# Kernel tuning notes

Measured on AMD Instinct MI355X. Metric: run time of the kernel, lower is better.

Reference implementation:

```python
import jax, jax.numpy as jnp
import numpy as np

INPUT_DIM = 1024
NUM_HEADS = 16


def setup_inputs() -> dict:
    key = jax.random.key(0)
    k1, k2, k3, k4, k5, k6, k7, k8 = jax.random.split(key, 8)
    bs, seq, dm = 2, 2048, INPUT_DIM
    scale = 1.0 / np.sqrt(dm)
    return {
        "input": jax.random.normal(k1, (bs, seq, dm), dtype=jnp.float32),
        "mask": jax.random.randint(k2, (bs, seq), 0, 2, dtype=jnp.int32),
        "Wq": jax.random.normal(k3, (dm, dm), dtype=jnp.float32) * scale,
        "bq": jax.random.normal(k4, (dm,), dtype=jnp.float32) * 0.01,
        "Wk": jax.random.normal(k5, (dm, dm), dtype=jnp.float32) * scale,
        "bk": jax.random.normal(k6, (dm,), dtype=jnp.float32) * 0.01,
        "Wv": jax.random.normal(k7, (dm, dm), dtype=jnp.float32) * scale,
        "bv": jax.random.normal(k8, (dm,), dtype=jnp.float32) * 0.01,
    }


def reference(input, mask, Wq, bq, Wk, bk, Wv, bv):
    bs, seq, dm = input.shape
    h = NUM_HEADS
    d = dm // h
    # projections: x @ W^T + b (torch Linear convention)
    Q = (input @ Wq.T + bq).reshape(bs, seq, h, d).transpose(0, 2, 1, 3)
    K = (input @ Wk.T + bk).reshape(bs, seq, h, d).transpose(0, 2, 1, 3)
    V = (input @ Wv.T + bv).reshape(bs, seq, h, d).transpose(0, 2, 1, 3)
    # raw scores [bs, h, seq, seq]
    scores = jnp.einsum("bhqd,bhkd->bhqk", Q, K)
    m = mask.astype(jnp.float32).reshape(bs, 1, 1, seq)
    # mask_logits is applied BEFORE the 1/sqrt(d) scaling, as in source
    scores = scores * m + (1.0 - m) * (-1e30)
    scores = scores * (1.0 / np.sqrt(d))
    attn = jax.nn.softmax(scores, axis=-1)  # dropout = identity at eval
    out = jnp.einsum("bhqk,bhkd->bhqd", attn, V)
    return out.transpose(0, 2, 1, 3).reshape(bs, seq, dm)
```

## Files before the change

kernel.cpp:

```cpp
#include <hip/hip_runtime.h>
#include <stdint.h>
#include <stddef.h>

#define SEQ 2048
#define DM  1024
#define NH  16
#define BS  2

typedef __attribute__((ext_vector_type(8)))  __bf16 bf16x8;
typedef __attribute__((ext_vector_type(4)))  __bf16 bf16x4;
typedef __attribute__((ext_vector_type(4)))  float  floatx4;
typedef __attribute__((ext_vector_type(16))) float  floatx16;
typedef __attribute__((ext_vector_type(4)))  unsigned int uintx4;
typedef __attribute__((ext_vector_type(4)))  unsigned short ushortx4;

#if __has_builtin(__builtin_amdgcn_exp2f)
#define EXP2(x) __builtin_amdgcn_exp2f(x)
#else
#define EXP2(x) __expf((x) * 0.6931471805599453f)
#endif

#define QSCALE 0.18033688011112042f

#define GLDS(g, s) __builtin_amdgcn_global_load_lds( \
    (const __attribute__((address_space(1))) void*)(g), \
    (__attribute__((address_space(3))) void*)(s), 16, 0, 0)

__device__ inline unsigned short f2bf(float f) {
  union { float f; unsigned int u; } a; a.f = f;
  unsigned int u = a.u;
  return (unsigned short)((u + 0x7fffu + ((u >> 16) & 1u)) >> 16);
}

__device__ inline bf16x8 ldb8(const unsigned short* p) { return *(const bf16x8*)p; }

__global__ __launch_bounds__(256) void prep(
    const float* __restrict__ x, const float* __restrict__ wq,
    const float* __restrict__ wk, const float* __restrict__ wv,
    const int* __restrict__ mask,
    unsigned short* __restrict__ Xb, unsigned short* __restrict__ Wb,
    unsigned short* __restrict__ mb01) {
  const int bid = blockIdx.x, t = threadIdx.x;
  if (bid < 7168) {
    const float* src; unsigned short* dst; int base;
    if (bid < 4096)      { src = x;  dst = Xb;            base = bid; }
    else if (bid < 5120) { src = wq; dst = Wb;            base = bid - 4096; }
    else if (bid < 6144) { src = wk; dst = Wb + 1048576;  base = bid - 5120; }
    else                 { src = wv; dst = Wb + 2097152;  base = bid - 6144; }
    const int i = base * 256 + t;
    floatx4 v = ((const floatx4*)src)[i];
    ushortx4 o;
    o.x = f2bf(v.x); o.y = f2bf(v.y); o.z = f2bf(v.z); o.w = f2bf(v.w);
    ((ushortx4*)dst)[i] = o;
  } else {
    const int i = (bid - 7168) * 256 + t;
    mb01[i] = mask[i] ? 0x3F80 : 0;
  }
}

__global__ __launch_bounds__(256, 3) void gemm_qkv(
    const unsigned short* __restrict__ Xb, const unsigned short* __restrict__ Wb,
    const float* __restrict__ bq, const float* __restrict__ bk, const float* __restrict__ bv,
    const int* __restrict__ mask,
    unsigned short* __restrict__ Qb, unsigned short* __restrict__ Kb,
    unsigned short* __restrict__ Vt)
{
  __shared__ alignas(16) unsigned short LB[16384];
  const int t = threadIdx.x;
  const int w = t >> 6, l = t & 63;
  const int lm = l & 15, lq = l >> 4;
  const int z = blockIdx.z;
  const size_t m0 = (size_t)blockIdx.y * 128;
  const size_t n0 = (size_t)blockIdx.x * 128;
  const unsigned short* W = Wb + (size_t)z * (1024 * 1024);
  const float* bias = (z == 0) ? bq : ((z == 1) ? bk : bv);
  const float sc = (z == 0) ? QSCALE : 1.0f;

  const int c0 = t, c1 = 256 + t;
  const int row0 = c0 >> 2, row1 = c1 >> 2;
  const int kq0 = (c0 & 3) ^ ((row0 >> 1) & 3);
  const int kq1 = (c1 & 3) ^ ((row1 >> 1) & 3);
  const unsigned short* gA0 = Xb + (m0 + row0) * 1024 + kq0 * 8;
  const unsigned short* gA1 = Xb + (m0 + row1) * 1024 + kq1 * 8;
  const unsigned short* gB0 = W + (n0 + row0) * 1024 + kq0 * 8;
  const unsigned short* gB1 = W + (n0 + row1) * 1024 + kq1 * 8;
  const int la0 = (0 * 256 + w * 64) * 8;
  const int la1 = (1 * 256 + w * 64) * 8;

  const int wr = (w >> 1) * 64, wc = (w & 1) * 64;
  const int sw = (lq ^ ((lm >> 1) & 3)) * 8;
  floatx4 acc[4][4] = {};

  GLDS(gA0, LB + la0);
  GLDS(gA1, LB + la1);
  GLDS(gB0, LB + 8192 + la0);
  GLDS(gB1, LB + 8192 + la1);
  __syncthreads();

  for (int it = 0; it < 32; ++it) {
    const int cur = it & 1;
    if (it < 31) {
      const int kn = (it + 1) * 32;
      const int nb = (cur ^ 1) * 4096;
      GLDS(gA0 + kn, LB + nb + la0);
      GLDS(gA1 + kn, LB + nb + la1);
      GLDS(gB0 + kn, LB + 8192 + nb + la0);
      GLDS(gB1 + kn, LB + 8192 + nb + la1);
    }
    const unsigned short* Ab = LB + cur * 4096;
    const unsigned short* Bb = LB + 8192 + cur * 4096;
    bf16x8 af[4], bfr[4];
#pragma unroll
    for (int i = 0; i < 4; i++) af[i] = ldb8(Ab + (wr + i * 16 + lm) * 32 + sw);
#pragma unroll
    for (int j = 0; j < 4; j++) bfr[j] = ldb8(Bb + (wc + j * 16 + lm) * 32 + sw);
#pragma unroll
    for (int i = 0; i < 4; i++)
#pragma unroll
      for (int j = 0; j < 4; j++)
        acc[i][j] = __builtin_amdgcn_mfma_f32_16x16x32_bf16(af[i], bfr[j], acc[i][j], 0, 0, 0);
    __syncthreads();
  }

  if (z < 2) {
    unsigned short* dst = (z == 0) ? Qb : Kb;
#pragma unroll
    for (int j = 0; j < 4; j++) {
      const int ncol = (int)n0 + wc + j * 16 + lm;
      const float bval = bias[ncol];
#pragma unroll
      for (int i = 0; i < 4; i++)
#pragma unroll
        for (int r = 0; r < 4; r++) {
          const int mrow = (int)m0 + wr + i * 16 + lq * 4 + r;
          dst[(size_t)mrow * 1024 + ncol] = f2bf((acc[i][j][r] + bval) * sc);
        }
    }
  } else {
    float mk[4][4];
#pragma unroll
    for (int i = 0; i < 4; i++)
#pragma unroll
      for (int r = 0; r < 4; r++)
        mk[i][r] = (float)mask[(int)m0 + wr + i * 16 + lq * 4 + r];
#pragma unroll
    for (int j = 0; j < 4; j++) {
      const int nl = wc + j * 16 + lm;
      const float bval = bias[(int)n0 + nl];
#pragma unroll
      for (int i = 0; i < 4; i++)
#pragma unroll
        for (int r = 0; r < 4; r++) {
          const int ml = wr + i * 16 + lq * 4 + r;
          LB[nl * 128 + ((((ml >> 3) ^ (nl & 15)) * 8) | (ml & 7))] =
              f2bf((acc[i][j][r] + bval) * mk[i][r]);
        }
    }
    __syncthreads();
    const int nl = t >> 1, hf = t & 1;
    const int ncol = (int)n0 + nl;
    const int hh = ncol >> 6, dc = ncol & 63;
    const int bb = (int)(m0 >> 11);
    const int s0c = ((int)m0 & 2047) + hf * 64;
    unsigned short* dstp = Vt + (size_t)((bb * 16 + hh) * 64 + dc) * SEQ + s0c;
#pragma unroll
    for (int u = 0; u < 8; ++u) {
      const int phys = (hf * 8 + u) ^ (nl & 15);
      *(uintx4*)(dstp + u * 8) = *(const uintx4*)(LB + nl * 128 + phys * 8);
    }
  }
}

__global__ __launch_bounds__(256, 3) void attn(
    const unsigned short* __restrict__ Qb, const unsigned short* __restrict__ Kb,
    const unsigned short* __restrict__ Vt, const unsigned short* __restrict__ mb01,
    float* __restrict__ out)
{
  __shared__ alignas(16) unsigned short Klds[2][4096];
  __shared__ alignas(16) unsigned short Vlds[2][4096];
  __shared__ alignas(16) unsigned short Plds[4][2048];
  __shared__ alignas(16) unsigned short Mb[2048];

  const int t = threadIdx.x, w = t >> 6, l = t & 63;
  const int ln = l & 31, h = l >> 5;
  const int bid = blockIdx.x;
  const int pp = bid & 31;
  const int b = pp >> 4, head = pp & 15;
  const int q0w = (bid >> 5) * 128 + w * 32;
  const int hoff = head * 64;

  const int sr = l >> 3;
  const int gc = (l & 7) ^ sr;
  const unsigned short* gK[2]; const unsigned short* gV[2];
#pragma unroll
  for (int s2 = 0; s2 < 2; ++s2) {
    const int row = w * 16 + s2 * 8 + sr;
    gK[s2] = Kb + (size_t)(b * SEQ + row) * DM + hoff + gc * 8;
    gV[s2] = Vt + (size_t)((b * NH + head) * 64 + row) * SEQ + gc * 8;
  }

#pragma unroll
  for (int s2 = 0; s2 < 2; ++s2) {
    GLDS(gK[s2], &Klds[0][(w * 128 + s2 * 64) * 8]);
    GLDS(gV[s2], &Vlds[0][(w * 128 + s2 * 64) * 8]);
  }

  ((uintx4*)Mb)[t] = ((const uintx4*)(mb01 + b * SEQ))[t];

  const unsigned short* Qbase = Qb + (size_t)(b * SEQ + q0w + ln) * DM + hoff + h * 8;
  bf16x8 qf[4];
#pragma unroll
  for (int c = 0; c < 4; ++c) qf[c] = ldb8(Qbase + c * 16);

  const int cc = (ln >> 1) & 3, hb = h ^ (ln & 1);
  int xoff[4];
#pragma unroll
  for (int c = 0; c < 4; ++c) xoff[c] = (c ^ cc) * 16 + hb * 8;

  unsigned short* Pw = &Plds[w][ln * 64];
  floatx16 oacc[2] = {};
  floatx16 tacc = {};

  __syncthreads();

  for (int kt = 0; kt < 32; ++kt) {
    const int cur = kt & 1;
    if (kt < 31) {
      const int k0n = (kt + 1) * 64;
#pragma unroll
      for (int s2 = 0; s2 < 2; ++s2) {
        GLDS(gK[s2] + (size_t)k0n * DM, &Klds[cur ^ 1][(w * 128 + s2 * 64) * 8]);
        GLDS(gV[s2] + k0n,              &Vlds[cur ^ 1][(w * 128 + s2 * 64) * 8]);
      }
    }
    const unsigned short* Kc = &Klds[cur][ln * 64];
    const unsigned short* Vc = &Vlds[cur][ln * 64];

    bf16x8 kfr[8], vfr[8];
#pragma unroll
    for (int i = 0; i < 8; ++i) {
      kfr[i] = ldb8(Kc + (i >> 2) * 2048 + xoff[i & 3]);
      vfr[i] = ldb8(Vc + (i >> 2) * 2048 + xoff[i & 3]);
    }

    floatx16 s[2] = {};
#pragma unroll
    for (int c = 0; c < 4; ++c) {
      s[0] = __builtin_amdgcn_mfma_f32_32x32x16_bf16(kfr[c],     qf[c], s[0], 0, 0, 0);
      s[1] = __builtin_amdgcn_mfma_f32_32x32x16_bf16(kfr[4 + c], qf[c], s[1], 0, 0, 0);
    }

#pragma unroll
    for (int kb = 0; kb < 2; ++kb)
#pragma unroll
      for (int g = 0; g < 4; ++g) {
        bf16x4 pk;
#pragma unroll
        for (int r = 0; r < 4; ++r) pk[r] = (__bf16)EXP2(s[kb][g * 4 + r]);
        *(bf16x4*)(Pw + ((4 * kb + g) ^ (ln & 7)) * 8 + h * 4) = pk;
      }

    bf16x8 pf[4];
#pragma unroll
    for (int c = 0; c < 4; ++c) pf[c] = ldb8(Pw + xoff[c]);

    const int k0 = kt * 64;
#pragma unroll
    for (int c = 0; c < 4; ++c) {
      const bf16x8 mfr = ldb8(Mb + k0 + c * 16 + h * 8);
      tacc = __builtin_amdgcn_mfma_f32_32x32x16_bf16(pf[c], mfr, tacc, 0, 0, 0);
    }

#pragma unroll
    for (int c = 0; c < 4; ++c) {
      oacc[0] = __builtin_amdgcn_mfma_f32_32x32x16_bf16(pf[c], vfr[c],     oacc[0], 0, 0, 0);
      oacc[1] = __builtin_amdgcn_mfma_f32_32x32x16_bf16(pf[c], vfr[4 + c], oacc[1], 0, 0, 0);
    }
    __syncthreads();
  }

  float* obase = out + (size_t)(b * SEQ + q0w) * DM + hoff;
#pragma unroll
  for (int r = 0; r < 16; ++r) {
    const int rq = (r & 3) + 8 * (r >> 2) + 4 * h;
    const float iv = __builtin_amdgcn_rcpf(tacc[r]);
    obase[(size_t)rq * DM + ln]      = oacc[0][r] * iv;
    obase[(size_t)rq * DM + 32 + ln] = oacc[1][r] * iv;
  }
}

extern "C" void kernel_launch(void* const* d_in, const int* in_sizes, int n_in,
                              void* d_out, int out_size, void* d_ws, size_t ws_size,
                              hipStream_t stream) {
  const float* x   = (const float*)d_in[0];
  const int*   msk = (const int*)d_in[1];
  const float* Wq  = (const float*)d_in[2];
  const float* bq  = (const float*)d_in[3];
  const float* Wk  = (const float*)d_in[4];
  const float* bk  = (const float*)d_in[5];
  const float* Wv  = (const float*)d_in[6];
  const float* bv  = (const float*)d_in[7];
  float* out = (float*)d_out;

  unsigned short* ws = (unsigned short*)d_ws;
  unsigned short* Xb = ws;
  unsigned short* Wb = Xb + (size_t)4096 * 1024;
  unsigned short* Qb = Wb + (size_t)3 * 1024 * 1024;
  unsigned short* Kb = Qb + (size_t)4096 * 1024;
  unsigned short* Vt = Kb + (size_t)4096 * 1024;
  unsigned short* mb01 = Vt + (size_t)4096 * 1024;

  prep<<<7184, 256, 0, stream>>>(x, Wq, Wk, Wv, msk, Xb, Wb, mb01);

  gemm_qkv<<<dim3(8, 32, 3), 256, 0, stream>>>(Xb, Wb, bq, bk, bv, msk, Qb, Kb, Vt);

  attn<<<512, 256, 0, stream>>>(Qb, Kb, Vt, mb01, out);
}
```

Baseline: 170.5 us.

## Software-pipeline QK^T one tile ahead with triple-buffered K/V LDS

Moves the attention loop to a three-stage K/V LDS ring and starts loads two tiles ahead. The QK^T MFMAs for the next tile are issued in the same iteration as the exp/P store and the PV MFMAs of the current tile, so matrix work can overlap the transcendental and LDS phases. K and V fragments are now read from LDS right before use rather than in one batch. In exchange, LDS use grows, launch bounds drop from 3 to 2 blocks per CU, register pressure rises from the extra score accumulators, and the last iteration does one wasted QK^T on a stale buffer.

```diff
diff --git a/kernel.cpp b/kernel.cpp
--- a/kernel.cpp
+++ b/kernel.cpp
@@ -171,13 +171,13 @@
   }
 }
 
-__global__ __launch_bounds__(256, 3) void attn(
+__global__ __launch_bounds__(256, 2) void attn(
     const unsigned short* __restrict__ Qb, const unsigned short* __restrict__ Kb,
     const unsigned short* __restrict__ Vt, const unsigned short* __restrict__ mb01,
     float* __restrict__ out)
 {
-  __shared__ alignas(16) unsigned short Klds[2][4096];
-  __shared__ alignas(16) unsigned short Vlds[2][4096];
+  __shared__ alignas(16) unsigned short Klds[3][4096];
+  __shared__ alignas(16) unsigned short Vlds[3][4096];
   __shared__ alignas(16) unsigned short Plds[4][2048];
   __shared__ alignas(16) unsigned short Mb[2048];
 
@@ -201,8 +201,10 @@
 
 #pragma unroll
   for (int s2 = 0; s2 < 2; ++s2) {
-    GLDS(gK[s2], &Klds[0][(w * 128 + s2 * 64) * 8]);
-    GLDS(gV[s2], &Vlds[0][(w * 128 + s2 * 64) * 8]);
+    GLDS(gK[s2],                  &Klds[0][(w * 128 + s2 * 64) * 8]);
+    GLDS(gV[s2],                  &Vlds[0][(w * 128 + s2 * 64) * 8]);
+    GLDS(gK[s2] + (size_t)64 * DM, &Klds[1][(w * 128 + s2 * 64) * 8]);
+    GLDS(gV[s2] + 64,              &Vlds[1][(w * 128 + s2 * 64) * 8]);
   }
 
   ((uintx4*)Mb)[t] = ((const uintx4*)(mb01 + b * SEQ))[t];
@@ -223,31 +225,33 @@
 
   __syncthreads();
 
+  floatx16 scur[2] = {};
+#pragma unroll
+  for (int c = 0; c < 4; ++c) {
+    const unsigned short* Kc = &Klds[0][ln * 64];
+    scur[0] = __builtin_amdgcn_mfma_f32_32x32x16_bf16(ldb8(Kc + xoff[c]),        qf[c], scur[0], 0, 0, 0);
+    scur[1] = __builtin_amdgcn_mfma_f32_32x32x16_bf16(ldb8(Kc + 2048 + xoff[c]), qf[c], scur[1], 0, 0, 0);
+  }
+
+  int cur = 0, nxt = 1, fut = 2;
   for (int kt = 0; kt < 32; ++kt) {
-    const int cur = kt & 1;
-    if (kt < 31) {
-      const int k0n = (kt + 1) * 64;
+    if (kt < 30) {
+      const int k0n = (kt + 2) * 64;
 #pragma unroll
       for (int s2 = 0; s2 < 2; ++s2) {
-        GLDS(gK[s2] + (size_t)k0n * DM, &Klds[cur ^ 1][(w * 128 + s2 * 64) * 8]);
-        GLDS(gV[s2] + k0n,              &Vlds[cur ^ 1][(w * 128 + s2 * 64) * 8]);
+        GLDS(gK[s2] + (size_t)k0n * DM, &Klds[fut][(w * 128 + s2 * 64) * 8]);
+        GLDS(gV[s2] + k0n,              &Vlds[fut][(w * 128 + s2 * 64) * 8]);
       }
     }
-    const unsigned short* Kc = &Klds[cur][ln * 64];
-    const unsigned short* Vc = &Vlds[cur][ln * 64];
-
-    bf16x8 kfr[8], vfr[8];
-#pragma unroll
-    for (int i = 0; i < 8; ++i) {
-      kfr[i] = ldb8(Kc + (i >> 2) * 2048 + xoff[i & 3]);
-      vfr[i] = ldb8(Vc + (i >> 2) * 2048 + xoff[i & 3]);
-    }
-
-    floatx16 s[2] = {};
-#pragma unroll
-    for (int c = 0; c < 4; ++c) {
-      s[0] = __builtin_amdgcn_mfma_f32_32x32x16_bf16(kfr[c],     qf[c], s[0], 0, 0, 0);
-      s[1] = __builtin_amdgcn_mfma_f32_32x32x16_bf16(kfr[4 + c], qf[c], s[1], 0, 0, 0);
+
+    floatx16 snext[2] = {};
+    {
+      const unsigned short* Kc = &Klds[nxt][ln * 64];
+#pragma unroll
+      for (int c = 0; c < 4; ++c) {
+        snext[0] = __builtin_amdgcn_mfma_f32_32x32x16_bf16(ldb8(Kc + xoff[c]),        qf[c], snext[0], 0, 0, 0);
+        snext[1] = __builtin_amdgcn_mfma_f32_32x32x16_bf16(ldb8(Kc + 2048 + xoff[c]), qf[c], snext[1], 0, 0, 0);
+      }
     }
 
 #pragma unroll
@@ -256,7 +260,7 @@
       for (int g = 0; g < 4; ++g) {
         bf16x4 pk;
 #pragma unroll
-        for (int r = 0; r < 4; ++r) pk[r] = (__bf16)EXP2(s[kb][g * 4 + r]);
+        for (int r = 0; r < 4; ++r) pk[r] = (__bf16)EXP2(scur[kb][g * 4 + r]);
         *(bf16x4*)(Pw + ((4 * kb + g) ^ (ln & 7)) * 8 + h * 4) = pk;
       }
 
@@ -271,12 +275,18 @@
       tacc = __builtin_amdgcn_mfma_f32_32x32x16_bf16(pf[c], mfr, tacc, 0, 0, 0);
     }
 
-#pragma unroll
-    for (int c = 0; c < 4; ++c) {
-      oacc[0] = __builtin_amdgcn_mfma_f32_32x32x16_bf16(pf[c], vfr[c],     oacc[0], 0, 0, 0);
-      oacc[1] = __builtin_amdgcn_mfma_f32_32x32x16_bf16(pf[c], vfr[4 + c], oacc[1], 0, 0, 0);
-    }
+    {
+      const unsigned short* Vc = &Vlds[cur][ln * 64];
+#pragma unroll
+      for (int c = 0; c < 4; ++c) {
+        oacc[0] = __builtin_amdgcn_mfma_f32_32x32x16_bf16(pf[c], ldb8(Vc + xoff[c]),        oacc[0], 0, 0, 0);
+        oacc[1] = __builtin_amdgcn_mfma_f32_32x32x16_bf16(pf[c], ldb8(Vc + 2048 + xoff[c]), oacc[1], 0, 0, 0);
+      }
+    }
+
     __syncthreads();
+    scur[0] = snext[0]; scur[1] = snext[1];
+    const int tmp = cur; cur = nxt; nxt = fut; fut = tmp;
   }
 
   float* obase = out + (size_t)(b * SEQ + q0w) * DM + hoff;
```

New measurement: 164.5 us. -3.5%, faster.

## Halve attention block size and apply key mask elementwise before PV

Applied to the files above, without the earlier changes.

The attention kernel now runs 1024 blocks of two wavefronts (64 queries each) instead of 512 blocks of four. Each wave therefore loads twice as many K/V rows into shared memory per tile. The key mask becomes a float array that is multiplied into exp(s) while P is formed, so the row-sum MFMA uses a constant ones vector and the shared-memory mask copy is gone. The cost is that K/V tiles are reused by fewer queries, doubling global K/V traffic per query, and each block now issues extra global mask loads per tile.

```diff
diff --git a/kernel.cpp b/kernel.cpp
--- a/kernel.cpp
+++ b/kernel.cpp
@@ -39,7 +39,7 @@
     const float* __restrict__ wk, const float* __restrict__ wv,
     const int* __restrict__ mask,
     unsigned short* __restrict__ Xb, unsigned short* __restrict__ Wb,
-    unsigned short* __restrict__ mb01) {
+    float* __restrict__ maskf) {
   const int bid = blockIdx.x, t = threadIdx.x;
   if (bid < 7168) {
     const float* src; unsigned short* dst; int base;
@@ -54,7 +54,7 @@
     ((ushortx4*)dst)[i] = o;
   } else {
     const int i = (bid - 7168) * 256 + t;
-    mb01[i] = mask[i] ? 0x3F80 : 0;
+    maskf[i] = mask[i] ? 1.0f : 0.0f;
   }
 }
 
@@ -171,41 +171,38 @@
   }
 }
 
-__global__ __launch_bounds__(256, 3) void attn(
+__global__ __launch_bounds__(128, 2) void attn(
     const unsigned short* __restrict__ Qb, const unsigned short* __restrict__ Kb,
-    const unsigned short* __restrict__ Vt, const unsigned short* __restrict__ mb01,
+    const unsigned short* __restrict__ Vt, const float* __restrict__ maskf,
     float* __restrict__ out)
 {
   __shared__ alignas(16) unsigned short Klds[2][4096];
   __shared__ alignas(16) unsigned short Vlds[2][4096];
-  __shared__ alignas(16) unsigned short Plds[4][2048];
-  __shared__ alignas(16) unsigned short Mb[2048];
+  __shared__ alignas(16) unsigned short Plds[2][2048];
 
   const int t = threadIdx.x, w = t >> 6, l = t & 63;
   const int ln = l & 31, h = l >> 5;
   const int bid = blockIdx.x;
   const int pp = bid & 31;
   const int b = pp >> 4, head = pp & 15;
-  const int q0w = (bid >> 5) * 128 + w * 32;
+  const int q0w = (bid >> 5) * 64 + w * 32;
   const int hoff = head * 64;
 
   const int sr = l >> 3;
   const int gc = (l & 7) ^ sr;
-  const unsigned short* gK[2]; const unsigned short* gV[2];
-#pragma unroll
-  for (int s2 = 0; s2 < 2; ++s2) {
-    const int row = w * 16 + s2 * 8 + sr;
+  const unsigned short* gK[4]; const unsigned short* gV[4];
+#pragma unroll
+  for (int s2 = 0; s2 < 4; ++s2) {
+    const int row = w * 32 + s2 * 8 + sr;
     gK[s2] = Kb + (size_t)(b * SEQ + row) * DM + hoff + gc * 8;
     gV[s2] = Vt + (size_t)((b * NH + head) * 64 + row) * SEQ + gc * 8;
   }
 
 #pragma unroll
-  for (int s2 = 0; s2 < 2; ++s2) {
-    GLDS(gK[s2], &Klds[0][(w * 128 + s2 * 64) * 8]);
-    GLDS(gV[s2], &Vlds[0][(w * 128 + s2 * 64) * 8]);
-  }
-
-  ((uintx4*)Mb)[t] = ((const uintx4*)(mb01 + b * SEQ))[t];
+  for (int s2 = 0; s2 < 4; ++s2) {
+    GLDS(gK[s2], &Klds[0][(w * 4 + s2) * 512]);
+    GLDS(gV[s2], &Vlds[0][(w * 4 + s2) * 512]);
+  }
 
   const unsigned short* Qbase = Qb + (size_t)(b * SEQ + q0w + ln) * DM + hoff + h * 8;
   bf16x8 qf[4];
@@ -217,6 +214,11 @@
 #pragma unroll
   for (int c = 0; c < 4; ++c) xoff[c] = (c ^ cc) * 16 + hb * 8;
 
+  bf16x8 onef;
+#pragma unroll
+  for (int i = 0; i < 8; ++i) onef[i] = (__bf16)1.0f;
+
+  const float* mbase = maskf + b * SEQ;
   unsigned short* Pw = &Plds[w][ln * 64];
   floatx16 oacc[2] = {};
   floatx16 tacc = {};
@@ -228,9 +230,9 @@
     if (kt < 31) {
       const int k0n = (kt + 1) * 64;
 #pragma unroll
-      for (int s2 = 0; s2 < 2; ++s2) {
-        GLDS(gK[s2] + (size_t)k0n * DM, &Klds[cur ^ 1][(w * 128 + s2 * 64) * 8]);
-        GLDS(gV[s2] + k0n,              &Vlds[cur ^ 1][(w * 128 + s2 * 64) * 8]);
+      for (int s2 = 0; s2 < 4; ++s2) {
+        GLDS(gK[s2] + (size_t)k0n * DM, &Klds[cur ^ 1][(w * 4 + s2) * 512]);
+        GLDS(gV[s2] + k0n,              &Vlds[cur ^ 1][(w * 4 + s2) * 512]);
       }
     }
     const unsigned short* Kc = &Klds[cur][ln * 64];
@@ -250,13 +252,15 @@
       s[1] = __builtin_amdgcn_mfma_f32_32x32x16_bf16(kfr[4 + c], qf[c], s[1], 0, 0, 0);
     }
 
+    const int k0 = kt * 64;
 #pragma unroll
     for (int kb = 0; kb < 2; ++kb)
 #pragma unroll
       for (int g = 0; g < 4; ++g) {
+        const floatx4 mkv = *(const floatx4*)(mbase + k0 + kb * 32 + g * 8 + h * 4);
         bf16x4 pk;
 #pragma unroll
-        for (int r = 0; r < 4; ++r) pk[r] = (__bf16)EXP2(s[kb][g * 4 + r]);
+        for (int r = 0; r < 4; ++r) pk[r] = (__bf16)(EXP2(s[kb][g * 4 + r]) * mkv[r]);
         *(bf16x4*)(Pw + ((4 * kb + g) ^ (ln & 7)) * 8 + h * 4) = pk;
       }
 
@@ -264,12 +268,9 @@
 #pragma unroll
     for (int c = 0; c < 4; ++c) pf[c] = ldb8(Pw + xoff[c]);
 
-    const int k0 = kt * 64;
-#pragma unroll
-    for (int c = 0; c < 4; ++c) {
-      const bf16x8 mfr = ldb8(Mb + k0 + c * 16 + h * 8);
-      tacc = __builtin_amdgcn_mfma_f32_32x32x16_bf16(pf[c], mfr, tacc, 0, 0, 0);
-    }
+#pragma unroll
+    for (int c = 0; c < 4; ++c)
+      tacc = __builtin_amdgcn_mfma_f32_32x32x16_bf16(pf[c], onef, tacc, 0, 0, 0);
 
 #pragma unroll
     for (int c = 0; c < 4; ++c) {
@@ -308,11 +309,11 @@
   unsigned short* Qb = Wb + (size_t)3 * 1024 * 1024;
   unsigned short* Kb = Qb + (size_t)4096 * 1024;
   unsigned short* Vt = Kb + (size_t)4096 * 1024;
-  unsigned short* mb01 = Vt + (size_t)4096 * 1024;
-
-  prep<<<7184, 256, 0, stream>>>(x, Wq, Wk, Wv, msk, Xb, Wb, mb01);
+  float* maskf = (float*)(Vt + (size_t)4096 * 1024);
+
+  prep<<<7184, 256, 0, stream>>>(x, Wq, Wk, Wv, msk, Xb, Wb, maskf);
 
   gemm_qkv<<<dim3(8, 32, 3), 256, 0, stream>>>(Xb, Wb, bq, bk, bv, msk, Qb, Kb, Vt);
 
-  attn<<<512, 256, 0, stream>>>(Qb, Kb, Vt, mb01, out);
-}
+  attn<<<1024, 128, 0, stream>>>(Qb, Kb, Vt, maskf, out);
+}
```

Result: slower. 177.4 us (+4.1%).
